# Kernel optimization log

Hardware: AMD Instinct MI355X
Metric: run time of the kernel (lower is better)

The kernel has to match this reference:

```python
import jax, jax.numpy as jnp
import numpy as np

SHIFTS = [1, 3, 5, 7]
C = 16  # in_channels // 4
# -1 neighbor offsets for tmp1..tmp8 (dy, dx) in units of the dilation
OFFSETS = [(-1, -1), (-1, 0), (-1, 1), (0, 1), (1, 1), (1, 0), (1, -1), (0, -1)]


def setup_inputs() -> dict:
    key = jax.random.key(0)
    ks = jax.random.split(key, 32)
    d = {}
    d['cen'] = jax.random.normal(ks[0], (8, 64, 256, 256), jnp.float32)
    d['mas'] = jax.random.normal(ks[1], (8, 1, 256, 256), jnp.float32)
    d['in_conv_w'] = jax.random.normal(ks[2], (16, 64), jnp.float32) * 0.1
    d['in_conv_b'] = jax.random.normal(ks[3], (16,), jnp.float32) * 0.1
    for i, s in enumerate(SHIFTS):
        d[f'dw_w{s}'] = jax.random.normal(ks[4 + 2 * i], (16, 1, s, s), jnp.float32) * 0.1
        d[f'dw_b{s}'] = jax.random.normal(ks[5 + 2 * i], (16,), jnp.float32) * 0.1
    d['l1_w'] = jax.random.normal(ks[12], (4, 16, 4), jnp.float32) * 0.1
    d['l1_b'] = jax.random.normal(ks[13], (4, 16), jnp.float32) * 0.1
    d['l2_w'] = jax.random.normal(ks[14], (4, 16, 8), jnp.float32) * 0.1
    d['l2_b'] = jax.random.normal(ks[15], (4, 16), jnp.float32) * 0.1
    d['base_w'] = jax.random.normal(ks[16], (16, 4), jnp.float32) * 0.1
    d['bn_scale'] = jnp.ones((16,), jnp.float32)
    d['bn_bias'] = jnp.zeros((16,), jnp.float32)
    d['final_w'] = jax.random.normal(ks[17], (1, 16), jnp.float32) * 0.1
    d['final_b'] = jax.random.normal(ks[18], (1,), jnp.float32) * 0.1
    return d


def _dw_conv(x, w, b, pad):
    # depthwise conv, groups == channels
    y = jax.lax.conv_general_dilated(
        x, w, window_strides=(1, 1), padding=[(pad, pad), (pad, pad)],
        dimension_numbers=('NCHW', 'OIHW', 'NCHW'), feature_group_count=x.shape[1])
    return y + b[None, :, None, None]


def _shifted(x, dy, dx, d):
    # zero-padded shift: out(y,x) = in(y+dy, x+dx)
    H, W = x.shape[2], x.shape[3]
    p = jnp.pad(x, ((0, 0), (0, 0), (d, d), (d, d)))
    return p[:, :, d + dy:d + dy + H, d + dx:d + dx + W]


def _circ_shift(x, dw_w, dw_b, w1, b1, w2, b2, shift):
    x = _dw_conv(x, dw_w, dw_b, shift // 2)
    # tmp_k = x - x shifted by the k-th neighbor offset (dilation = shift)
    T = [x - _shifted(x, dy * shift, dx * shift, shift) for dy, dx in OFFSETS]
    # paired sums: S[k] = tmp_{k+1} + tmp_{k+5} (S repeats with period 4)
    S = [T[k] + T[k + 4] for k in range(4)]
    outs = []
    for k in range(8):  # fixed small structural loop
        feats = jnp.stack([S[(k + 1) % 4], S[(k + 3) % 4], S[(k + 2) % 4],
                           2.0 * T[(k + 4) % 8]], axis=2)  # (B,C,4,H,W)
        # grouped 1x1 conv (groups=C, 4C->C) == per-channel contraction over feature axis
        o = jnp.einsum('bcfhw,cf->bchw', feats, w1) + b1[None, :, None, None]
        outs.append(o * T[k])
    O = jnp.sort(jnp.stack(outs, axis=2), axis=2)  # (B,C,8,H,W) sorted over branch axis
    return jnp.einsum('bcfhw,cf->bchw', O, w2) + b2[None, :, None, None]


def reference(cen, mas, in_conv_w, in_conv_b, dw_w1, dw_b1, dw_w3, dw_b3,
              dw_w5, dw_b5, dw_w7, dw_b7, l1_w, l1_b, l2_w, l2_b,
              base_w, bn_scale, bn_bias, final_w, final_b):
    # in_conv: 1x1, in_channels -> C
    x = jnp.einsum('bihw,oi->bohw', cen, in_conv_w) + in_conv_b[None, :, None, None]
    dws = [(dw_w1, dw_b1), (dw_w3, dw_b3), (dw_w5, dw_b5), (dw_w7, dw_b7)]
    branches = [
        _circ_shift(x, dws[i][0], dws[i][1], l1_w[i], l1_b[i], l2_w[i], l2_b[i], SHIFTS[i])
        for i in range(len(SHIFTS))
    ]
    A = jnp.sort(jnp.stack(branches, axis=2), axis=2)  # (B,C,4,H,W)
    # out_conv: grouped 1x1 BaseConv (conv no-bias + BN(affine) + SiLU), then 1x1 -> 1, sigmoid
    y = jnp.einsum('bcfhw,cf->bchw', A, base_w)
    y = jax.nn.silu(y * bn_scale[None, :, None, None] + bn_bias[None, :, None, None])
    y = jnp.einsum('bchw,oc->bohw', y, final_w) + final_b[None, :, None, None]
    return jax.nn.sigmoid(y)
```

## Files before the change

### kernel.cpp

```cpp
#include <hip/hip_runtime.h>
#include <hip/hip_fp16.h>
#include <math.h>

#define HW 65536

typedef float v2f __attribute__((ext_vector_type(2), aligned(8)));
typedef _Float16 h2 __attribute__((ext_vector_type(2)));

__device__ __forceinline__ h2 uh(unsigned u) { return __builtin_bit_cast(h2, u); }
__device__ __forceinline__ unsigned hu(h2 v) { return __builtin_bit_cast(unsigned, v); }
__device__ __forceinline__ unsigned algn(unsigned lo, unsigned hi) {
    return (lo >> 16) | (hi << 16);
}

#define CEH(a, b) { h2 _t = __builtin_elementwise_min(a, b); \
                    b = __builtin_elementwise_max(a, b); a = _t; }

__device__ __forceinline__ void sort8_h2(h2* v) {
    CEH(v[0], v[1]); CEH(v[2], v[3]); CEH(v[4], v[5]); CEH(v[6], v[7]);
    CEH(v[0], v[2]); CEH(v[1], v[3]); CEH(v[4], v[6]); CEH(v[5], v[7]);
    CEH(v[1], v[2]); CEH(v[5], v[6]); CEH(v[0], v[4]); CEH(v[3], v[7]);
    CEH(v[1], v[5]); CEH(v[2], v[6]);
    CEH(v[1], v[4]); CEH(v[3], v[6]);
    CEH(v[2], v[4]); CEH(v[3], v[5]);
    CEH(v[3], v[4]);
}
__device__ __forceinline__ void sort4_h2(h2* v) {
    CEH(v[0], v[1]); CEH(v[2], v[3]); CEH(v[0], v[2]); CEH(v[1], v[3]); CEH(v[1], v[2]);
}

__global__ __launch_bounds__(256) void k_pack(const float* __restrict__ l1w,
                                              const float* __restrict__ l1b,
                                              const float* __restrict__ l2w,
                                              const float* __restrict__ l2b,
                                              const float* __restrict__ bw,
                                              const float* __restrict__ dw_w1,
                                              const float* __restrict__ dw_b1,
                                              const float* __restrict__ dw_w3,
                                              const float* __restrict__ dw_b3,
                                              const float* __restrict__ dw_w5,
                                              const float* __restrict__ dw_b5,
                                              const float* __restrict__ dw_w7,
                                              const float* __restrict__ dw_b7,
                                              unsigned* __restrict__ wtab) {
    for (int t = threadIdx.x; t < 3584; t += 256) {
        float v = 0.f;
        if (t < 1024) {
            int c = t >> 6, i = (t >> 4) & 3, j = t & 15;
            if (j < 3)        v = l1w[i * 64 + c * 4 + j];
            else if (j == 3)  v = 2.f * l1w[i * 64 + c * 4 + 3];
            else if (j == 4)  v = l1b[i * 16 + c];
            else if (j < 13)  v = l2w[i * 128 + c * 8 + (j - 5)];
            else if (j == 13) v = l2b[i * 16 + c];
        } else if (t < 1088) {
            v = bw[t - 1024];
        } else if (t >= 2048) {
            int c = (t - 2048) / 96, j = (t - 2048) - c * 96;
            if (j < 49)       v = dw_w7[c * 49 + j];
            else if (j < 74)  v = dw_w5[c * 25 + (j - 49)];
            else if (j < 83)  v = dw_w3[c * 9 + (j - 74)];
            else if (j == 83) v = dw_w1[c];
            else if (j == 84) v = dw_b1[c];
            else if (j == 85) v = dw_b3[c];
            else if (j == 86) v = dw_b5[c];
            else if (j == 87) v = dw_b7[c];
        }
        unsigned hs = (unsigned)__half_as_ushort(__float2half(v));
        wtab[t] = hs * 0x10001u;
    }
}

__global__ __launch_bounds__(256, 4) void k_inconv(const float* __restrict__ cen,
                                                   const float* __restrict__ w,
                                                   const float* __restrict__ bias,
                                                   __half* __restrict__ xh) {
    __shared__ float wl[1040];
    int tid = threadIdx.x;
    for (int t = tid; t < 1024; t += 256) wl[t] = w[(t & 15) * 64 + (t >> 4)];
    if (tid < 16) wl[1024 + tid] = bias[tid];
    __syncthreads();

    int pr = blockIdx.x * 256 + tid;
    int b_ = pr >> 15;
    int hw = (pr & 32767) * 2;
    const float* src = cen + (size_t)(b_ * 64) * HW + hw;

    v2f acc[16];
#pragma unroll
    for (int o = 0; o < 16; o++) { float bv = wl[1024 + o]; v2f t = {bv, bv}; acc[o] = t; }

#pragma unroll 8
    for (int i = 0; i < 64; i++) {
        v2f xv = *(const v2f*)(src + (size_t)i * HW);
        const float4* wq = (const float4*)&wl[i * 16];
#pragma unroll
        for (int g = 0; g < 4; g++) {
            float4 f = wq[g];
            acc[g * 4 + 0] += xv * f.x;
            acc[g * 4 + 1] += xv * f.y;
            acc[g * 4 + 2] += xv * f.z;
            acc[g * 4 + 3] += xv * f.w;
        }
    }
    __half* dst = xh + (size_t)(b_ * 16) * HW + hw;
#pragma unroll
    for (int o = 0; o < 16; o++)
        *(__half2*)(dst + (size_t)o * HW) = __floats2half2_rn(acc[o].x, acc[o].y);
}

#define LXS 44
#define CTS 42
#define CTP (78 * CTS)

template<int S, int PAD>
__device__ __forceinline__ void branch_pair(const unsigned* pl, int R, int g,
                                            const unsigned* wt, h2* outA, h2* outB) {
    const int D = 2 * g + (7 - S) / 2 + PAD;
    const int L = (S + 3) / 2;
    const unsigned* pt = pl + (R + 7 - S) * CTS + D;
    const unsigned* pm = pl + (R + 7) * CTS + D;
    const unsigned* pb = pl + (R + 7 + S) * CTS + D;
    unsigned ut[2 * L], um[2 * L], ub[2 * L];
#pragma unroll
    for (int k = 0; k < L; k++) {
        *(uint2*)&ut[2 * k] = *(const uint2*)(pt + 2 * k);
        *(uint2*)&um[2 * k] = *(const uint2*)(pm + 2 * k);
        *(uint2*)&ub[2 * k] = *(const uint2*)(pb + 2 * k);
    }
#pragma unroll
    for (int dw = 0; dw < 2; dw++) {
        h2 n0 = uh(ut[dw]);
        h2 n1 = uh(algn(ut[(S - 1) / 2 + dw], ut[(S + 1) / 2 + dw]));
        h2 n2 = uh(ut[S + dw]);
        h2 n7 = uh(um[dw]);
        h2 ct = uh(algn(um[(S - 1) / 2 + dw], um[(S + 1) / 2 + dw]));
        h2 n3 = uh(um[S + dw]);
        h2 n6 = uh(ub[dw]);
        h2 n5 = uh(algn(ub[(S - 1) / 2 + dw], ub[(S + 1) / 2 + dw]));
        h2 n4 = uh(ub[S + dw]);

        h2 T[8];
        T[0] = ct - n0; T[1] = ct - n1; T[2] = ct - n2; T[3] = ct - n3;
        T[4] = ct - n4; T[5] = ct - n5; T[6] = ct - n6; T[7] = ct - n7;
        h2 Sm[4];
#pragma unroll
        for (int k = 0; k < 4; k++) Sm[k] = T[k] + T[k + 4];

        h2 w10 = uh(wt[0]), w11 = uh(wt[1]), w12 = uh(wt[2]);
        h2 w13x2 = uh(wt[3]), bb1 = uh(wt[4]);

        h2 R4[4];
#pragma unroll
        for (int mm = 0; mm < 4; mm++) {
            h2 r = Sm[(mm + 2) & 3] * w12 + bb1;
            r = Sm[(mm + 3) & 3] * w11 + r;
            r = Sm[(mm + 1) & 3] * w10 + r;
            R4[mm] = r;
        }
        h2 h8[8];
#pragma unroll
        for (int k = 0; k < 8; k++)
            h8[k] = (T[(k + 4) & 7] * w13x2 + R4[k & 3]) * T[k];
        sort8_h2(h8);

        h2 acc = uh(wt[13]);
#pragma unroll
        for (int k = 0; k < 8; k++) acc += h8[k] * uh(wt[5 + k]);
        if (dw == 0) *outA = acc; else *outB = acc;
    }
}

__device__ __forceinline__ unsigned tail_px(h2* bh, const unsigned* __restrict__ wtab,
                                            int c, float bsc, float bbi) {
    sort4_h2(bh);
    h2 yv = bh[0] * uh(wtab[1024 + (c << 2)]);
#pragma unroll
    for (int k = 1; k < 4; k++) yv = bh[k] * uh(wtab[1024 + (c << 2) + k]) + yv;
    float zx = fmaf((float)yv.x, bsc, bbi);
    float zy = fmaf((float)yv.y, bsc, bbi);
    float sx = zx / (1.f + __expf(-zx));
    float sy = zy / (1.f + __expf(-zy));
    return __builtin_bit_cast(unsigned, __floats2half2_rn(sx, sy));
}

__global__ __launch_bounds__(1024, 8) void k_fused(const __half* __restrict__ xh,
    const unsigned* __restrict__ wtab,
    const float* __restrict__ bns, const float* __restrict__ bnb,
    __half* __restrict__ y16) {

    const int by  = blockIdx.y;
    const int c   = by & 15;
    const int ty0 = (blockIdx.x >> 2) * 64;
    const int tx0 = (blockIdx.x & 3) * 64;
    const int tid = threadIdx.x;

    __shared__ unsigned lxh[84 * LXS];
    __shared__ unsigned convt[4 * CTP];

    {
        const unsigned* xp32 = (const unsigned*)(xh + (size_t)by * HW);
        for (int t = tid; t < 84 * 21; t += 1024) {
            int r = t / 21, j = t - r * 21;
            int gy = ty0 - 10 + r;
            int gp = tx0 - 10 + 4 * j;
            unsigned v0 = 0, v1 = 0;
            if ((unsigned)gy < 256u) {
                const unsigned* rp = xp32 + (gy << 7);
                if ((unsigned)gp < 256u)       v0 = rp[gp >> 1];
                if ((unsigned)(gp + 2) < 256u) v1 = rp[(gp >> 1) + 1];
            }
            uint2 st = {v0, v1};
            *(uint2*)&lxh[r * LXS + 2 * j] = st;
        }
    }
    __syncthreads();

    {
        const unsigned* dwc = wtab + 2048 + c * 96;
        for (int u = tid; u < 78 * 20; u += 1024) {
            int row = u / 20;
            int g   = u - row * 20;
            h2 a7A = {0, 0}, a7B = {0, 0}, a5A = {0, 0}, a5B = {0, 0};
            h2 a3A = {0, 0}, a3B = {0, 0}, a1A = {0, 0}, a1B = {0, 0};
#pragma unroll
            for (int a = 0; a < 7; a++) {
                const unsigned* rp = lxh + (row + a) * LXS + 2 * g;
                uint2 w0 = *(const uint2*)rp;
                uint2 w1 = *(const uint2*)(rp + 2);
                uint2 w2 = *(const uint2*)(rp + 4);
                unsigned u0 = w0.x, u1 = w0.y, u2 = w1.x, u3 = w1.y, u4 = w2.x;
                h2 E[9] = {uh(u0), uh(algn(u0, u1)), uh(u1), uh(algn(u1, u2)),
                           uh(u2), uh(algn(u2, u3)), uh(u3), uh(algn(u3, u4)), uh(u4)};
#pragma unroll
                for (int b = 0; b < 7; b++) {
                    h2 wv = uh(dwc[a * 7 + b]);
                    a7A = E[b] * wv + a7A;  a7B = E[b + 2] * wv + a7B;
                }
                if (a >= 1 && a <= 5) {
#pragma unroll
                    for (int b = 0; b < 5; b++) {
                        h2 wv = uh(dwc[49 + (a - 1) * 5 + b]);
                        a5A = E[b + 1] * wv + a5A;  a5B = E[b + 3] * wv + a5B;
                    }
                }
                if (a >= 2 && a <= 4) {
#pragma unroll
                    for (int b = 0; b < 3; b++) {
                        h2 wv = uh(dwc[74 + (a - 2) * 3 + b]);
                        a3A = E[b + 2] * wv + a3A;  a3B = E[b + 4] * wv + a3B;
                    }
                }
                if (a == 3) {
                    h2 wv = uh(dwc[83]);
                    a1A = E[3] * wv;  a1B = E[5] * wv;
                }
            }
            int iy = ty0 - 7 + row;
            bool rin = (unsigned)iy < 256u;
            int ix0 = tx0 - 7 + 4 * g;
            unsigned mA = (rin && (unsigned)ix0 < 256u ? 0x0000FFFFu : 0u)
                        | (rin && (unsigned)(ix0 + 1) < 256u ? 0xFFFF0000u : 0u);
            unsigned mB = (rin && (unsigned)(ix0 + 2) < 256u ? 0x0000FFFFu : 0u)
                        | (rin && (unsigned)(ix0 + 3) < 256u ? 0xFFFF0000u : 0u);
            int o = row * CTS + 2 * g;
            uint2 s3 = {hu(a3A + uh(dwc[85])) & mA, hu(a3B + uh(dwc[85])) & mB};
            uint2 s7 = {hu(a7A + uh(dwc[87])) & mA, hu(a7B + uh(dwc[87])) & mB};
            *(uint2*)&convt[CTP + o]     = s3;
            *(uint2*)&convt[3 * CTP + o] = s7;
            convt[o + 1]                 = hu(a1A + uh(dwc[84])) & mA;
            convt[o + 2]                 = hu(a1B + uh(dwc[84])) & mB;
            convt[2 * CTP + o + 1]       = hu(a5A + uh(dwc[86])) & mA;
            convt[2 * CTP + o + 2]       = hu(a5B + uh(dwc[86])) & mB;
        }
    }
    __syncthreads();

    const int R = tid >> 4;
    const int g = tid & 15;

    h2 bhA[4], bhB[4];
    branch_pair<1, 1>(convt,           R, g, wtab + ((c << 2) + 0) * 16, &bhA[0], &bhB[0]);
    branch_pair<3, 0>(convt + CTP,     R, g, wtab + ((c << 2) + 1) * 16, &bhA[1], &bhB[1]);
    branch_pair<5, 1>(convt + 2 * CTP, R, g, wtab + ((c << 2) + 2) * 16, &bhA[2], &bhB[2]);
    branch_pair<7, 0>(convt + 3 * CTP, R, g, wtab + ((c << 2) + 3) * 16, &bhA[3], &bhB[3]);

    const float bsc = bns[c], bbi = bnb[c];
    unsigned r0 = tail_px(bhA, wtab, c, bsc, bbi);
    unsigned r1 = tail_px(bhB, wtab, c, bsc, bbi);
    uint2 st = {r0, r1};
    *(uint2*)&y16[(size_t)by * HW + (ty0 + R) * 256 + tx0 + 4 * g] = st;
}

__global__ __launch_bounds__(256) void k_final(const __half* __restrict__ y16,
                                               const float* __restrict__ fw,
                                               const float* __restrict__ fb,
                                               float* __restrict__ out) {
    long t  = (long)blockIdx.x * 256 + threadIdx.x;
    long p0 = t * 2;
    int  b  = (int)(p0 >> 16);
    int  hw = (int)(p0 & 65535);

    float accx = fb[0], accy = fb[0];
#pragma unroll
    for (int cc = 0; cc < 16; cc++) {
        __half2 h = *(const __half2*)(y16 + (size_t)(b * 16 + cc) * HW + hw);
        float2 v = __half22float2(h);
        float wv = fw[cc];
        accx = fmaf(v.x, wv, accx);
        accy = fmaf(v.y, wv, accy);
    }
    float2 r;
    r.x = 1.f / (1.f + __expf(-accx));
    r.y = 1.f / (1.f + __expf(-accy));
    *(float2*)(out + p0) = r;
}

extern "C" void kernel_launch(void* const* d_in, const int* in_sizes, int n_in,
                              void* d_out, int out_size, void* d_ws, size_t ws_size,
                              hipStream_t stream) {
    (void)in_sizes; (void)n_in; (void)out_size; (void)ws_size;
    const float* cen   = (const float*)d_in[0];
    const float* in_w  = (const float*)d_in[2];
    const float* in_b  = (const float*)d_in[3];
    const float* dw_w1 = (const float*)d_in[4];
    const float* dw_b1 = (const float*)d_in[5];
    const float* dw_w3 = (const float*)d_in[6];
    const float* dw_b3 = (const float*)d_in[7];
    const float* dw_w5 = (const float*)d_in[8];
    const float* dw_b5 = (const float*)d_in[9];
    const float* dw_w7 = (const float*)d_in[10];
    const float* dw_b7 = (const float*)d_in[11];
    const float* l1w   = (const float*)d_in[12];
    const float* l1b   = (const float*)d_in[13];
    const float* l2w   = (const float*)d_in[14];
    const float* l2b   = (const float*)d_in[15];
    const float* bw    = (const float*)d_in[16];
    const float* bns   = (const float*)d_in[17];
    const float* bnb   = (const float*)d_in[18];
    const float* fw    = (const float*)d_in[19];
    const float* fb    = (const float*)d_in[20];

    __half*   xh   = (__half*)d_ws;
    unsigned* wtab = (unsigned*)((char*)d_ws + (size_t)16777216);
    __half*   y16  = (__half*)((char*)d_ws + (size_t)16777216 + 16384);
    float*    out  = (float*)d_out;

    k_pack<<<1, 256, 0, stream>>>(l1w, l1b, l2w, l2b, bw,
                                  dw_w1, dw_b1, dw_w3, dw_b3,
                                  dw_w5, dw_b5, dw_w7, dw_b7, wtab);
    k_inconv<<<1024, 256, 0, stream>>>(cen, in_w, in_b, xh);
    k_fused<<<dim3(16, 128), 1024, 0, stream>>>(xh, wtab, bns, bnb, y16);
    k_final<<<1024, 256, 0, stream>>>(y16, fw, fb, out);
}
```

Baseline: 333.1 us.

## Prepack in_conv weights in global memory, unroll fused loops, widen final kernel

The in_conv weight transpose moves into the pack kernel, so k_inconv reads weights straight from global memory (scalar, uniform loads) and no longer stages them in shared memory or synchronises. The fused kernel's load and depthwise-conv loops are unrolled into a fixed two-iteration form through a helper, and the final kernel handles four pixels per thread with wider loads and stores on half the grid. The aim is less shared-memory traffic, fewer barriers and less loop overhead. The cost is heavier reliance on scalar cache or constant loads in the in_conv kernel.

```diff
diff --git a/kernel.cpp b/kernel.cpp
--- a/kernel.cpp
+++ b/kernel.cpp
@@ -42,6 +42,8 @@
                                               const float* __restrict__ dw_b5,
                                               const float* __restrict__ dw_w7,
                                               const float* __restrict__ dw_b7,
+                                              const float* __restrict__ in_w,
+                                              const float* __restrict__ in_b,
                                               unsigned* __restrict__ wtab) {
     for (int t = threadIdx.x; t < 3584; t += 256) {
         float v = 0.f;
@@ -68,39 +70,30 @@
         unsigned hs = (unsigned)__half_as_ushort(__float2half(v));
         wtab[t] = hs * 0x10001u;
     }
-}
-
-__global__ __launch_bounds__(256, 4) void k_inconv(const float* __restrict__ cen,
-                                                   const float* __restrict__ w,
-                                                   const float* __restrict__ bias,
-                                                   __half* __restrict__ xh) {
-    __shared__ float wl[1040];
-    int tid = threadIdx.x;
-    for (int t = tid; t < 1024; t += 256) wl[t] = w[(t & 15) * 64 + (t >> 4)];
-    if (tid < 16) wl[1024 + tid] = bias[tid];
-    __syncthreads();
-
-    int pr = blockIdx.x * 256 + tid;
+    float* wtf = (float*)(wtab + 4096);
+    for (int t = threadIdx.x; t < 1040; t += 256) {
+        wtf[t] = (t < 1024) ? in_w[(t & 15) * 64 + (t >> 4)] : in_b[t - 1024];
+    }
+}
+
+__global__ __launch_bounds__(256) void k_inconv(const float* __restrict__ cen,
+                                                const float* __restrict__ wtf,
+                                                __half* __restrict__ xh) {
+    int pr = blockIdx.x * 256 + threadIdx.x;
     int b_ = pr >> 15;
     int hw = (pr & 32767) * 2;
     const float* src = cen + (size_t)(b_ * 64) * HW + hw;
 
     v2f acc[16];
 #pragma unroll
-    for (int o = 0; o < 16; o++) { float bv = wl[1024 + o]; v2f t = {bv, bv}; acc[o] = t; }
+    for (int o = 0; o < 16; o++) { float bv = wtf[1024 + o]; v2f t = {bv, bv}; acc[o] = t; }
 
 #pragma unroll 8
     for (int i = 0; i < 64; i++) {
         v2f xv = *(const v2f*)(src + (size_t)i * HW);
-        const float4* wq = (const float4*)&wl[i * 16];
-#pragma unroll
-        for (int g = 0; g < 4; g++) {
-            float4 f = wq[g];
-            acc[g * 4 + 0] += xv * f.x;
-            acc[g * 4 + 1] += xv * f.y;
-            acc[g * 4 + 2] += xv * f.z;
-            acc[g * 4 + 3] += xv * f.w;
-        }
+#pragma unroll
+        for (int o = 0; o < 16; o++)
+            acc[o] += xv * wtf[i * 16 + o];
     }
     __half* dst = xh + (size_t)(b_ * 16) * HW + hw;
 #pragma unroll
@@ -183,6 +176,63 @@
     return __builtin_bit_cast(unsigned, __floats2half2_rn(sx, sy));
 }
 
+__device__ __forceinline__ void conv_group(const unsigned* lxh, unsigned* convt,
+                                           const unsigned* dwc, int ty0, int tx0, int u) {
+    int row = u / 20;
+    int g   = u - row * 20;
+    h2 a7A = {0, 0}, a7B = {0, 0}, a5A = {0, 0}, a5B = {0, 0};
+    h2 a3A = {0, 0}, a3B = {0, 0}, a1A = {0, 0}, a1B = {0, 0};
+#pragma unroll
+    for (int a = 0; a < 7; a++) {
+        const unsigned* rp = lxh + (row + a) * LXS + 2 * g;
+        uint2 w0 = *(const uint2*)rp;
+        uint2 w1 = *(const uint2*)(rp + 2);
+        uint2 w2 = *(const uint2*)(rp + 4);
+        unsigned u0 = w0.x, u1 = w0.y, u2 = w1.x, u3 = w1.y, u4 = w2.x;
+        h2 E[9] = {uh(u0), uh(algn(u0, u1)), uh(u1), uh(algn(u1, u2)),
+                   uh(u2), uh(algn(u2, u3)), uh(u3), uh(algn(u3, u4)), uh(u4)};
+#pragma unroll
+        for (int b = 0; b < 7; b++) {
+            h2 wv = uh(dwc[a * 7 + b]);
+            a7A = E[b] * wv + a7A;  a7B = E[b + 2] * wv + a7B;
+        }
+        if (a >= 1 && a <= 5) {
+#pragma unroll
+            for (int b = 0; b < 5; b++) {
+                h2 wv = uh(dwc[49 + (a - 1) * 5 + b]);
+                a5A = E[b + 1] * wv + a5A;  a5B = E[b + 3] * wv + a5B;
+            }
+        }
+        if (a >= 2 && a <= 4) {
+#pragma unroll
+            for (int b = 0; b < 3; b++) {
+                h2 wv = uh(dwc[74 + (a - 2) * 3 + b]);
+                a3A = E[b + 2] * wv + a3A;  a3B = E[b + 4] * wv + a3B;
+            }
+        }
+        if (a == 3) {
+            h2 wv = uh(dwc[83]);
+            a1A = E[3] * wv;  a1B = E[5] * wv;
+        }
+    }
+    int iy = ty0 - 7 + row;
+    bool rin = (unsigned)iy < 256u;
+    int ix0 = tx0 - 7 + 4 * g;
+    unsigned mA = (rin && (unsigned)ix0 < 256u ? 0x0000FFFFu : 0u)
+                | (rin && (unsigned)(ix0 + 1) < 256u ? 0xFFFF0000u : 0u);
+    unsigned mB = (rin && (unsigned)(ix0 + 2) < 256u ? 0x0000FFFFu : 0u)
+                | (rin && (unsigned)(ix0 + 3) < 256u ? 0xFFFF0000u : 0u);
+    int o = row * CTS + 2 * g;
+    uint2 s3 = {hu(a3A + uh(dwc[85])) & mA, hu(a3B + uh(dwc[85])) & mB};
+    uint2 s7 = {hu(a7A + uh(dwc[87])) & mA, hu(a7B + uh(dwc[87])) & mB};
+    *(uint2*)&convt[CTP + o]     = s3;
+    *(uint2*)&convt[3 * CTP + o] = s7;
+    convt[o + 1]                 = hu(a1A + uh(dwc[84])) & mA;
+    convt[o + 2]                 = hu(a1B + uh(dwc[84])) & mB;
+    convt[2 * CTP + o + 1]       = hu(a5A + uh(dwc[86])) & mA;
+    convt[2 * CTP + o + 2]       = hu(a5B + uh(dwc[86])) & mB;
+}
+
 __global__ __launch_bounds__(1024, 8) void k_fused(const __half* __restrict__ xh,
     const unsigned* __restrict__ wtab,
     const float* __restrict__ bns, const float* __restrict__ bnb,
@@ -199,79 +249,31 @@
 
     {
         const unsigned* xp32 = (const unsigned*)(xh + (size_t)by * HW);
-        for (int t = tid; t < 84 * 21; t += 1024) {
-            int r = t / 21, j = t - r * 21;
-            int gy = ty0 - 10 + r;
-            int gp = tx0 - 10 + 4 * j;
-            unsigned v0 = 0, v1 = 0;
-            if ((unsigned)gy < 256u) {
-                const unsigned* rp = xp32 + (gy << 7);
-                if ((unsigned)gp < 256u)       v0 = rp[gp >> 1];
-                if ((unsigned)(gp + 2) < 256u) v1 = rp[(gp >> 1) + 1];
+#pragma unroll
+        for (int it = 0; it < 2; it++) {
+            int t = tid + it * 1024;
+            if (it == 0 || t < 84 * 21) {
+                int r = t / 21, j = t - r * 21;
+                int gy = ty0 - 10 + r;
+                int gp = tx0 - 10 + 4 * j;
+                unsigned v0 = 0, v1 = 0;
+                if ((unsigned)gy < 256u) {
+                    const unsigned* rp = xp32 + (gy << 7);
+                    if ((unsigned)gp < 256u)       v0 = rp[gp >> 1];
+                    if ((unsigned)(gp + 2) < 256u) v1 = rp[(gp >> 1) + 1];
+                }
+                uint2 st = {v0, v1};
+                *(uint2*)&lxh[r * LXS + 2 * j] = st;
             }
-            uint2 st = {v0, v1};
-            *(uint2*)&lxh[r * LXS + 2 * j] = st;
         }
     }
     __syncthreads();
 
     {
         const unsigned* dwc = wtab + 2048 + c * 96;
-        for (int u = tid; u < 78 * 20; u += 1024) {
-            int row = u / 20;
-            int g   = u - row * 20;
-            h2 a7A = {0, 0}, a7B = {0, 0}, a5A = {0, 0}, a5B = {0, 0};
-            h2 a3A = {0, 0}, a3B = {0, 0}, a1A = {0, 0}, a1B = {0, 0};
-#pragma unroll
-            for (int a = 0; a < 7; a++) {
-                const unsigned* rp = lxh + (row + a) * LXS + 2 * g;
-                uint2 w0 = *(const uint2*)rp;
-                uint2 w1 = *(const uint2*)(rp + 2);
-                uint2 w2 = *(const uint2*)(rp + 4);
-                unsigned u0 = w0.x, u1 = w0.y, u2 = w1.x, u3 = w1.y, u4 = w2.x;
-                h2 E[9] = {uh(u0), uh(algn(u0, u1)), uh(u1), uh(algn(u1, u2)),
-                           uh(u2), uh(algn(u2, u3)), uh(u3), uh(algn(u3, u4)), uh(u4)};
-#pragma unroll
-                for (int b = 0; b < 7; b++) {
-                    h2 wv = uh(dwc[a * 7 + b]);
-                    a7A = E[b] * wv + a7A;  a7B = E[b + 2] * wv + a7B;
-                }
-                if (a >= 1 && a <= 5) {
-#pragma unroll
-                    for (int b = 0; b < 5; b++) {
-                        h2 wv = uh(dwc[49 + (a - 1) * 5 + b]);
-                        a5A = E[b + 1] * wv + a5A;  a5B = E[b + 3] * wv + a5B;
-                    }
-                }
-                if (a >= 2 && a <= 4) {
-#pragma unroll
-                    for (int b = 0; b < 3; b++) {
-                        h2 wv = uh(dwc[74 + (a - 2) * 3 + b]);
-                        a3A = E[b + 2] * wv + a3A;  a3B = E[b + 4] * wv + a3B;
-                    }
-                }
-                if (a == 3) {
-                    h2 wv = uh(dwc[83]);
-                    a1A = E[3] * wv;  a1B = E[5] * wv;
-                }
-            }
-            int iy = ty0 - 7 + row;
-            bool rin = (unsigned)iy < 256u;
-            int ix0 = tx0 - 7 + 4 * g;
-            unsigned mA = (rin && (unsigned)ix0 < 256u ? 0x0000FFFFu : 0u)
-                        | (rin && (unsigned)(ix0 + 1) < 256u ? 0xFFFF0000u : 0u);
-            unsigned mB = (rin && (unsigned)(ix0 + 2) < 256u ? 0x0000FFFFu : 0u)
-                        | (rin && (unsigned)(ix0 + 3) < 256u ? 0xFFFF0000u : 0u);
-            int o = row * CTS + 2 * g;
-            uint2 s3 = {hu(a3A + uh(dwc[85])) & mA, hu(a3B + uh(dwc[85])) & mB};
-            uint2 s7 = {hu(a7A + uh(dwc[87])) & mA, hu(a7B + uh(dwc[87])) & mB};
-            *(uint2*)&convt[CTP + o]     = s3;
-            *(uint2*)&convt[3 * CTP + o] = s7;
-            convt[o + 1]                 = hu(a1A + uh(dwc[84])) & mA;
-            convt[o + 2]                 = hu(a1B + uh(dwc[84])) & mB;
-            convt[2 * CTP + o + 1]       = hu(a5A + uh(dwc[86])) & mA;
-            convt[2 * CTP + o + 2]       = hu(a5B + uh(dwc[86])) & mB;
-        }
+        conv_group(lxh, convt, dwc, ty0, tx0, tid);
+        if (tid + 1024 < 78 * 20)
+            conv_group(lxh, convt, dwc, ty0, tx0, tid + 1024);
     }
     __syncthreads();
 
@@ -296,23 +298,29 @@
                                                const float* __restrict__ fb,
                                                float* __restrict__ out) {
     long t  = (long)blockIdx.x * 256 + threadIdx.x;
-    long p0 = t * 2;
+    long p0 = t * 4;
     int  b  = (int)(p0 >> 16);
     int  hw = (int)(p0 & 65535);
 
-    float accx = fb[0], accy = fb[0];
+    float bv = fb[0];
+    float a0 = bv, a1 = bv, a2 = bv, a3 = bv;
 #pragma unroll
     for (int cc = 0; cc < 16; cc++) {
-        __half2 h = *(const __half2*)(y16 + (size_t)(b * 16 + cc) * HW + hw);
-        float2 v = __half22float2(h);
+        uint2 u = *(const uint2*)(y16 + (size_t)(b * 16 + cc) * HW + hw);
+        float2 v0 = __half22float2(__builtin_bit_cast(__half2, u.x));
+        float2 v1 = __half22float2(__builtin_bit_cast(__half2, u.y));
         float wv = fw[cc];
-        accx = fmaf(v.x, wv, accx);
-        accy = fmaf(v.y, wv, accy);
-    }
-    float2 r;
-    r.x = 1.f / (1.f + __expf(-accx));
-    r.y = 1.f / (1.f + __expf(-accy));
-    *(float2*)(out + p0) = r;
+        a0 = fmaf(v0.x, wv, a0);
+        a1 = fmaf(v0.y, wv, a1);
+        a2 = fmaf(v1.x, wv, a2);
+        a3 = fmaf(v1.y, wv, a3);
+    }
+    float4 r;
+    r.x = 1.f / (1.f + __expf(-a0));
+    r.y = 1.f / (1.f + __expf(-a1));
+    r.z = 1.f / (1.f + __expf(-a2));
+    r.w = 1.f / (1.f + __expf(-a3));
+    *(float4*)(out + p0) = r;
 }
 
 extern "C" void kernel_launch(void* const* d_in, const int* in_sizes, int n_in,
@@ -342,13 +350,14 @@
 
     __half*   xh   = (__half*)d_ws;
     unsigned* wtab = (unsigned*)((char*)d_ws + (size_t)16777216);
-    __half*   y16  = (__half*)((char*)d_ws + (size_t)16777216 + 16384);
+    float*    wtf  = (float*)((char*)d_ws + (size_t)16777216 + 16384);
+    __half*   y16  = (__half*)((char*)d_ws + (size_t)16777216 + 16384 + 8192);
     float*    out  = (float*)d_out;
 
     k_pack<<<1, 256, 0, stream>>>(l1w, l1b, l2w, l2b, bw,
                                   dw_w1, dw_b1, dw_w3, dw_b3,
-                                  dw_w5, dw_b5, dw_w7, dw_b7, wtab);
-    k_inconv<<<1024, 256, 0, stream>>>(cen, in_w, in_b, xh);
+                                  dw_w5, dw_b5, dw_w7, dw_b7, in_w, in_b, wtab);
+    k_inconv<<<1024, 256, 0, stream>>>(cen, wtf, xh);
     k_fused<<<dim3(16, 128), 1024, 0, stream>>>(xh, wtab, bns, bnb, y16);
-    k_final<<<1024, 256, 0, stream>>>(y16, fw, fb, out);
-}
+    k_final<<<512, 256, 0, stream>>>(y16, fw, fb, out);
+}
```

After: 332.5 us. Within noise of the previous version (-0.2%).
